# Kernel tuning notes

Hardware: AMD Instinct MI355X
Metric: run time of the kernel (lower is better)

## Reference

```python
import jax, jax.numpy as jnp
import numpy as np

T, E, H = 65536, 512, 512  # seq_len, embedding_size, hidden_size (kernel_size=2)


def setup_inputs() -> dict:
    key = jax.random.key(0)
    k1, k2 = jax.random.split(key)
    x = jax.random.normal(k1, (T, E), dtype=jnp.float32)
    # nn.Linear(2*E, 3*H): weight [3H, 2E], bias [3H]. Store transposed for x @ W.
    W = jax.random.normal(k2, (2 * E, 3 * H), dtype=jnp.float32) * 0.02
    b = jnp.zeros((3 * H,), dtype=jnp.float32)
    return {"input": x, "W": W, "b": b}


def reference(input, W, b):
    x = input
    t, e = x.shape
    h_dim = W.shape[1] // 3
    # Shift input by one step (zero-padded) and concat: conv over kernel_size=2 window.
    x_prev = jnp.concatenate([jnp.zeros((1, e), x.dtype), x[:-1]], axis=0)  # [T, E]
    gates = jnp.concatenate([x, x_prev], axis=1) @ W + b  # [T, 3H]
    z = jnp.tanh(gates[:, :h_dim])                # cell candidate
    f = jax.nn.sigmoid(gates[:, h_dim:2 * h_dim])  # forget gate
    o = jax.nn.sigmoid(gates[:, 2 * h_dim:])       # output gate

    # fo-pool recurrence: c_t = f_t * c_{t-1} + (1 - f_t) * z_t ; h_t = o_t * c_t
    def step(c, zfo):
        z_t, f_t, o_t = zfo
        c_new = f_t * c + (1.0 - f_t) * z_t
        return c_new, (c_new, o_t * c_new)

    c0 = jnp.zeros((h_dim,), x.dtype)
    _, (cells, hiddens) = jax.lax.scan(step, c0, (z, f, o))
    # Match torch: (hidden_temp [T,H], h [1,H], c [1,H])
    return hiddens, hiddens[-1:], cells[-1:]
```

## Files before the change

kernel.cpp:

```cpp
#include <hip/hip_runtime.h>


#define T_LEN 65536
#define H3    1536
#define LC    64
#define NCHUNK 1024

typedef float f32x4 __attribute__((ext_vector_type(4)));
typedef short bf16x8 __attribute__((ext_vector_type(8)));

__device__ __forceinline__ unsigned short f2bf(float f) {
    unsigned int x = __builtin_bit_cast(unsigned int, f);
    x += 0x7fffu + ((x >> 16) & 1u);
    return (unsigned short)(x >> 16);
}
__device__ __forceinline__ float bf2f(unsigned short u) {
    return __builtin_bit_cast(float, ((unsigned int)u) << 16);
}
__device__ __forceinline__ float fsig(float x) {
    return __builtin_amdgcn_rcpf(1.f + __builtin_amdgcn_exp2f(-1.44269504f * x));
}
__device__ __forceinline__ float ftanh(float x) {
    return 2.f * __builtin_amdgcn_rcpf(1.f + __builtin_amdgcn_exp2f(-2.88539008f * x)) - 1.f;
}

__device__ __forceinline__ void gload_lds16(const void* g, void* l) {
    __builtin_amdgcn_global_load_lds((const __attribute__((address_space(1))) void*)g,
                                     (__attribute__((address_space(3))) void*)l, 16, 0, 0);
}

__global__ void prep_x(const float* __restrict__ x, unsigned short* __restrict__ xp) {
    const long long nq = (512LL + (long long)T_LEN * 512) / 4;
    for (long long q = (long long)blockIdx.x * blockDim.x + threadIdx.x; q < nq;
         q += (long long)gridDim.x * blockDim.x) {
        ushort4 u;
        if (q < 128) {
            u.x = 0; u.y = 0; u.z = 0; u.w = 0;
        } else {
            const float4 v = *reinterpret_cast<const float4*>(x + q * 4 - 512);
            u.x = f2bf(v.x); u.y = f2bf(v.y); u.z = f2bf(v.z); u.w = f2bf(v.w);
        }
        *reinterpret_cast<ushort4*>(xp + q * 4) = u;
    }
}

__global__ void prep_w(const float* __restrict__ W, unsigned short* __restrict__ Wt) {
    const int n_el = 1024 * H3;
    for (int i = blockIdx.x * blockDim.x + threadIdx.x; i < n_el;
         i += gridDim.x * blockDim.x) {
        const int k = i / H3, n = i - k * H3;
        Wt[n * 1024 + k] = f2bf(W[i]);
    }
}

__global__ __launch_bounds__(256, 2) void gemm_gates(
    const unsigned short* __restrict__ xp,
    const unsigned short* __restrict__ Wt,
    const float* __restrict__ bias,
    unsigned short* __restrict__ zfo)
{
    __shared__ unsigned short Alds[3][128 * 32];
    __shared__ unsigned short Blds[3][256 * 32];

    const int tid  = threadIdx.x;
    const int lane = tid & 63;
    const int w    = tid >> 6;
    const int wm   = w >> 1, wn = w & 1;

    const int flat = blockIdx.y * gridDim.x + blockIdx.x;
    const int idx  = (flat & 7) * 384 + (flat >> 3);
    const int nb   = (idx % 6) * 256;
    const long long t0 = (long long)(idx / 6) * 128;

    const int srow_l = lane >> 2;
    const int scol   = (((lane & 3) ^ ((lane >> 3) & 3)) * 8);

    const unsigned short* gA = xp + (t0 + w * 16 + srow_l) * 512 + 512 + scol;
    const unsigned short* gB = Wt + (long long)(nb + w * 16 + srow_l) * 1024 + scol;

    auto stage = [&](unsigned short* Al, unsigned short* Bl) {
        gload_lds16(gA,              Al + (w * 16) * 32);
        gload_lds16(gA + 64 * 512,   Al + (64 + w * 16) * 32);
        gload_lds16(gB,              Bl + (w * 16) * 32);
        gload_lds16(gB + 64 * 1024,  Bl + (64 + w * 16) * 32);
        gload_lds16(gB + 128 * 1024, Bl + (128 + w * 16) * 32);
        gload_lds16(gB + 192 * 1024, Bl + (192 + w * 16) * 32);
    };

    const int arow  = lane & 15;
    const int swzco = (((lane >> 4) ^ ((arow >> 1) & 3)) * 8);

    f32x4 acc[4][8] = {};

    auto compute = [&](const unsigned short* Al, const unsigned short* Bl) {
        bf16x8 af[4], bfr[8];
        #pragma unroll
        for (int m = 0; m < 4; ++m)
            af[m] = *reinterpret_cast<const bf16x8*>(Al + (wm * 64 + m * 16 + arow) * 32 + swzco);
        #pragma unroll
        for (int n = 0; n < 8; ++n)
            bfr[n] = *reinterpret_cast<const bf16x8*>(Bl + (wn * 128 + n * 16 + arow) * 32 + swzco);
        #pragma unroll
        for (int n = 0; n < 8; ++n)
            #pragma unroll
            for (int m = 0; m < 4; ++m)
                acc[m][n] = __builtin_amdgcn_mfma_f32_16x16x32_bf16(af[m], bfr[n], acc[m][n], 0, 0, 0);
    };

    stage(Alds[0], Blds[0]); gA += 32; gB += 32;
    stage(Alds[1], Blds[1]); gA += 32; gB += 32;
    asm volatile("s_waitcnt vmcnt(6)" ::: "memory");
    __builtin_amdgcn_s_barrier();

    for (int kt = 0; kt < 30; kt += 3) {
        {
            stage(Alds[2], Blds[2]);
            gA += (kt + 2 == 15) ? -992 : 32;  gB += 32;
            compute(Alds[0], Blds[0]);
            asm volatile("s_waitcnt vmcnt(6)" ::: "memory");
            __builtin_amdgcn_s_barrier();
        }
        {
            stage(Alds[0], Blds[0]);
            gA += (kt + 3 == 15) ? -992 : 32;  gB += 32;
            compute(Alds[1], Blds[1]);
            asm volatile("s_waitcnt vmcnt(6)" ::: "memory");
            __builtin_amdgcn_s_barrier();
        }
        {
            stage(Alds[1], Blds[1]);
            gA += (kt + 4 == 15) ? -992 : 32;  gB += 32;
            compute(Alds[2], Blds[2]);
            asm volatile("s_waitcnt vmcnt(6)" ::: "memory");
            __builtin_amdgcn_s_barrier();
        }
    }
    compute(Alds[0], Blds[0]);
    asm volatile("s_waitcnt vmcnt(0)" ::: "memory");
    __builtin_amdgcn_s_barrier();
    compute(Alds[1], Blds[1]);

    const int cls = nb >> 9;
    #pragma unroll
    for (int n = 0; n < 8; ++n) {
        const int col = nb + wn * 128 + n * 16 + arow;
        const float bn_ = bias[col];
        #pragma unroll
        for (int m = 0; m < 4; ++m) {
            const long long row0 = t0 + wm * 64 + m * 16 + (lane >> 4) * 4;
            #pragma unroll
            for (int j = 0; j < 4; ++j) {
                float v = acc[m][n][j] + bn_;
                v = (cls == 0) ? ftanh(v) : fsig(v);
                zfo[(row0 + j) * H3 + col] = f2bf(v);
            }
        }
    }
}

__global__ void scan_pass1(const unsigned short* __restrict__ zfo,
                           float* __restrict__ P, float* __restrict__ L) {
    const int chunk = blockIdx.x;
    const int c4    = threadIdx.x;
    const unsigned short* base = zfo + (long long)chunk * LC * H3 + c4 * 4;
    float c[4] = {0.f, 0.f, 0.f, 0.f};
    float p[4] = {1.f, 1.f, 1.f, 1.f};
    for (int t = 0; t < LC; ++t) {
        const unsigned short* row = base + t * H3;
        const ushort4 uz = *reinterpret_cast<const ushort4*>(row);
        const ushort4 uf = *reinterpret_cast<const ushort4*>(row + 512);
        const float z[4] = {bf2f(uz.x), bf2f(uz.y), bf2f(uz.z), bf2f(uz.w)};
        const float f[4] = {bf2f(uf.x), bf2f(uf.y), bf2f(uf.z), bf2f(uf.w)};
        #pragma unroll
        for (int j = 0; j < 4; ++j) {
            c[j] = fmaf(f[j], c[j] - z[j], z[j]);
            p[j] *= f[j];
        }
    }
    #pragma unroll
    for (int j = 0; j < 4; ++j) {
        P[chunk * 512 + c4 * 4 + j] = p[j];
        L[chunk * 512 + c4 * 4 + j] = c[j];
    }
}

__global__ __launch_bounds__(1024) void scan_pass2(
    const float* __restrict__ P, const float* __restrict__ L,
    float* __restrict__ carry, float* __restrict__ out) {
    const int ch = blockIdx.x;
    const int k  = threadIdx.x;
    __shared__ float sP[1024], sL[1024];
    float p = P[k * 512 + ch];
    float l = L[k * 512 + ch];
    sP[k] = p; sL[k] = l;
    __syncthreads();
    for (int d = 1; d < 1024; d <<= 1) {
        float pp = 1.f, ll = 0.f;
        if (k >= d) { pp = sP[k - d]; ll = sL[k - d]; }
        __syncthreads();
        l = fmaf(p, ll, l);
        p = p * pp;
        sP[k] = p; sL[k] = l;
        __syncthreads();
    }
    carry[k * 512 + ch] = (k == 0) ? 0.f : sL[k - 1];
    if (k == 1023) out[(long long)T_LEN * 512 + 512 + ch] = l;
}

__global__ void scan_pass3(const unsigned short* __restrict__ zfo,
                           const float* __restrict__ carry,
                           float* __restrict__ out) {
    const int chunk = blockIdx.x;
    const int c4    = threadIdx.x;
    const unsigned short* base = zfo + (long long)chunk * LC * H3 + c4 * 4;
    float c[4], h[4] = {0.f, 0.f, 0.f, 0.f};
    #pragma unroll
    for (int j = 0; j < 4; ++j) c[j] = carry[chunk * 512 + c4 * 4 + j];
    float4* outp = reinterpret_cast<float4*>(out + (long long)chunk * LC * 512) + c4;
    for (int t = 0; t < LC; ++t) {
        const unsigned short* row = base + t * H3;
        const ushort4 uz = *reinterpret_cast<const ushort4*>(row);
        const ushort4 uf = *reinterpret_cast<const ushort4*>(row + 512);
        const ushort4 uo = *reinterpret_cast<const ushort4*>(row + 1024);
        const float z[4] = {bf2f(uz.x), bf2f(uz.y), bf2f(uz.z), bf2f(uz.w)};
        const float f[4] = {bf2f(uf.x), bf2f(uf.y), bf2f(uf.z), bf2f(uf.w)};
        const float o[4] = {bf2f(uo.x), bf2f(uo.y), bf2f(uo.z), bf2f(uo.w)};
        #pragma unroll
        for (int j = 0; j < 4; ++j) {
            c[j] = fmaf(f[j], c[j] - z[j], z[j]);
            h[j] = o[j] * c[j];
        }
        float4 hv; hv.x = h[0]; hv.y = h[1]; hv.z = h[2]; hv.w = h[3];
        outp[t * 128] = hv;
    }
    if (chunk == NCHUNK - 1) {
        #pragma unroll
        for (int j = 0; j < 4; ++j)
            out[(long long)T_LEN * 512 + c4 * 4 + j] = h[j];
    }
}

extern "C" void kernel_launch(void* const* d_in, const int* in_sizes, int n_in,
                              void* d_out, int out_size, void* d_ws, size_t ws_size,
                              hipStream_t stream) {
    const float* x = (const float*)d_in[0];
    const float* W = (const float*)d_in[1];
    const float* b = (const float*)d_in[2];
    float* out = (float*)d_out;

    char* ws = (char*)d_ws;
    unsigned short* xp  = (unsigned short*)(ws);
    unsigned short* Wt  = (unsigned short*)(ws + 67110912LL);
    unsigned short* zfo = (unsigned short*)(ws + 70256640LL);
    float* P     = (float*)(ws);
    float* L     = (float*)(ws + 4194304LL);
    float* carry = (float*)(ws + 8388608LL);

    prep_x<<<4096, 256, 0, stream>>>(x, xp);
    prep_w<<<768, 256, 0, stream>>>(W, Wt);

    dim3 gg(H3 / 256, T_LEN / 128, 1);
    gemm_gates<<<gg, 256, 0, stream>>>(xp, Wt, b, zfo);

    scan_pass1<<<NCHUNK, 128, 0, stream>>>(zfo, P, L);
    scan_pass2<<<512, 1024, 0, stream>>>(P, L, carry, out);
    scan_pass3<<<NCHUNK, 128, 0, stream>>>(zfo, carry, out);
}
```

Measured before the change: 382.9 us.

## Merge prep kernels, halve scan chunk count, use nontemporal output stores

Combines the x and W conversion kernels into one launch to save a kernel launch. Doubles the scan chunk length to 128, which halves the number of chunks and the depth of the pass-2 carry scan, at the cost of fewer blocks in passes 1 and 3. Output stores in pass 3 become nontemporal to avoid polluting the cache with the large hidden-state output. Workspace offsets for P, L and carry are shrunk to match.

```diff
diff --git a/kernel.cpp b/kernel.cpp
--- a/kernel.cpp
+++ b/kernel.cpp
@@ -3,8 +3,8 @@
 
 #define T_LEN 65536
 #define H3    1536
-#define LC    64
-#define NCHUNK 1024
+#define LC    128
+#define NCHUNK 512
 
 typedef float f32x4 __attribute__((ext_vector_type(4)));
 typedef short bf16x8 __attribute__((ext_vector_type(8)));
@@ -29,27 +29,33 @@
                                      (__attribute__((address_space(3))) void*)l, 16, 0, 0);
 }
 
-__global__ void prep_x(const float* __restrict__ x, unsigned short* __restrict__ xp) {
-    const long long nq = (512LL + (long long)T_LEN * 512) / 4;
-    for (long long q = (long long)blockIdx.x * blockDim.x + threadIdx.x; q < nq;
-         q += (long long)gridDim.x * blockDim.x) {
-        ushort4 u;
-        if (q < 128) {
-            u.x = 0; u.y = 0; u.z = 0; u.w = 0;
-        } else {
-            const float4 v = *reinterpret_cast<const float4*>(x + q * 4 - 512);
-            u.x = f2bf(v.x); u.y = f2bf(v.y); u.z = f2bf(v.z); u.w = f2bf(v.w);
-        }
-        *reinterpret_cast<ushort4*>(xp + q * 4) = u;
-    }
-}
-
-__global__ void prep_w(const float* __restrict__ W, unsigned short* __restrict__ Wt) {
-    const int n_el = 1024 * H3;
-    for (int i = blockIdx.x * blockDim.x + threadIdx.x; i < n_el;
-         i += gridDim.x * blockDim.x) {
-        const int k = i / H3, n = i - k * H3;
-        Wt[n * 1024 + k] = f2bf(W[i]);
+#define VM6()   asm volatile("s_waitcnt vmcnt(6)" ::: "memory")
+#define VM0()   asm volatile("s_waitcnt vmcnt(0)" ::: "memory")
+#define BARX()  __builtin_amdgcn_s_barrier()
+
+__global__ void prep_all(const float* __restrict__ x, const float* __restrict__ W,
+                         unsigned short* __restrict__ xp, unsigned short* __restrict__ Wt) {
+    if (blockIdx.x < 768) {
+        const int n_el = 1024 * H3;
+        for (int i = blockIdx.x * blockDim.x + threadIdx.x; i < n_el;
+             i += 768 * blockDim.x) {
+            const int k = i / H3, n = i - k * H3;
+            Wt[n * 1024 + k] = f2bf(W[i]);
+        }
+    } else {
+        const int bx = blockIdx.x - 768;
+        const long long nq = (512LL + (long long)T_LEN * 512) / 4;
+        for (long long q = (long long)bx * blockDim.x + threadIdx.x; q < nq;
+             q += 4096LL * blockDim.x) {
+            ushort4 u;
+            if (q < 128) {
+                u.x = 0; u.y = 0; u.z = 0; u.w = 0;
+            } else {
+                const float4 v = *reinterpret_cast<const float4*>(x + q * 4 - 512);
+                u.x = f2bf(v.x); u.y = f2bf(v.y); u.z = f2bf(v.z); u.w = f2bf(v.w);
+            }
+            *reinterpret_cast<ushort4*>(xp + q * 4) = u;
+        }
     }
 }
 
@@ -109,35 +115,35 @@
 
     stage(Alds[0], Blds[0]); gA += 32; gB += 32;
     stage(Alds[1], Blds[1]); gA += 32; gB += 32;
-    asm volatile("s_waitcnt vmcnt(6)" ::: "memory");
-    __builtin_amdgcn_s_barrier();
+    VM6();
+    BARX();
 
     for (int kt = 0; kt < 30; kt += 3) {
         {
             stage(Alds[2], Blds[2]);
             gA += (kt + 2 == 15) ? -992 : 32;  gB += 32;
             compute(Alds[0], Blds[0]);
-            asm volatile("s_waitcnt vmcnt(6)" ::: "memory");
-            __builtin_amdgcn_s_barrier();
+            VM6();
+            BARX();
         }
         {
             stage(Alds[0], Blds[0]);
             gA += (kt + 3 == 15) ? -992 : 32;  gB += 32;
             compute(Alds[1], Blds[1]);
-            asm volatile("s_waitcnt vmcnt(6)" ::: "memory");
-            __builtin_amdgcn_s_barrier();
+            VM6();
+            BARX();
         }
         {
             stage(Alds[1], Blds[1]);
             gA += (kt + 4 == 15) ? -992 : 32;  gB += 32;
             compute(Alds[2], Blds[2]);
-            asm volatile("s_waitcnt vmcnt(6)" ::: "memory");
-            __builtin_amdgcn_s_barrier();
+            VM6();
+            BARX();
         }
     }
     compute(Alds[0], Blds[0]);
-    asm volatile("s_waitcnt vmcnt(0)" ::: "memory");
-    __builtin_amdgcn_s_barrier();
+    VM0();
+    BARX();
     compute(Alds[1], Blds[1]);
 
     const int cls = nb >> 9;
@@ -184,17 +190,17 @@
     }
 }
 
-__global__ __launch_bounds__(1024) void scan_pass2(
+__global__ __launch_bounds__(512) void scan_pass2(
     const float* __restrict__ P, const float* __restrict__ L,
     float* __restrict__ carry, float* __restrict__ out) {
     const int ch = blockIdx.x;
     const int k  = threadIdx.x;
-    __shared__ float sP[1024], sL[1024];
+    __shared__ float sP[NCHUNK], sL[NCHUNK];
     float p = P[k * 512 + ch];
     float l = L[k * 512 + ch];
     sP[k] = p; sL[k] = l;
     __syncthreads();
-    for (int d = 1; d < 1024; d <<= 1) {
+    for (int d = 1; d < NCHUNK; d <<= 1) {
         float pp = 1.f, ll = 0.f;
         if (k >= d) { pp = sP[k - d]; ll = sL[k - d]; }
         __syncthreads();
@@ -204,7 +210,7 @@
         __syncthreads();
     }
     carry[k * 512 + ch] = (k == 0) ? 0.f : sL[k - 1];
-    if (k == 1023) out[(long long)T_LEN * 512 + 512 + ch] = l;
+    if (k == NCHUNK - 1) out[(long long)T_LEN * 512 + 512 + ch] = l;
 }
 
 __global__ void scan_pass3(const unsigned short* __restrict__ zfo,
@@ -216,7 +222,7 @@
     float c[4], h[4] = {0.f, 0.f, 0.f, 0.f};
     #pragma unroll
     for (int j = 0; j < 4; ++j) c[j] = carry[chunk * 512 + c4 * 4 + j];
-    float4* outp = reinterpret_cast<float4*>(out + (long long)chunk * LC * 512) + c4;
+    f32x4* outp = reinterpret_cast<f32x4*>(out + (long long)chunk * LC * 512) + c4;
     for (int t = 0; t < LC; ++t) {
         const unsigned short* row = base + t * H3;
         const ushort4 uz = *reinterpret_cast<const ushort4*>(row);
@@ -230,8 +236,8 @@
             c[j] = fmaf(f[j], c[j] - z[j], z[j]);
             h[j] = o[j] * c[j];
         }
-        float4 hv; hv.x = h[0]; hv.y = h[1]; hv.z = h[2]; hv.w = h[3];
-        outp[t * 128] = hv;
+        f32x4 hv = {h[0], h[1], h[2], h[3]};
+        __builtin_nontemporal_store(hv, outp + t * 128);
     }
     if (chunk == NCHUNK - 1) {
         #pragma unroll
@@ -253,16 +259,15 @@
     unsigned short* Wt  = (unsigned short*)(ws + 67110912LL);
     unsigned short* zfo = (unsigned short*)(ws + 70256640LL);
     float* P     = (float*)(ws);
-    float* L     = (float*)(ws + 4194304LL);
-    float* carry = (float*)(ws + 8388608LL);
-
-    prep_x<<<4096, 256, 0, stream>>>(x, xp);
-    prep_w<<<768, 256, 0, stream>>>(W, Wt);
+    float* L     = (float*)(ws + 2097152LL);
+    float* carry = (float*)(ws + 4194304LL);
+
+    prep_all<<<768 + 4096, 256, 0, stream>>>(x, W, xp, Wt);
 
     dim3 gg(H3 / 256, T_LEN / 128, 1);
     gemm_gates<<<gg, 256, 0, stream>>>(xp, Wt, b, zfo);
 
     scan_pass1<<<NCHUNK, 128, 0, stream>>>(zfo, P, L);
-    scan_pass2<<<512, 1024, 0, stream>>>(P, L, carry, out);
+    scan_pass2<<<512, NCHUNK, 0, stream>>>(P, L, carry, out);
     scan_pass3<<<NCHUNK, 128, 0, stream>>>(zfo, carry, out);
 }
```

New measurement: 369.8 us. 3.4% less time.
